# Performance work log

Hardware: AMD Instinct MI355X
Metric: run time of the kernel (lower is better)

Reference implementation:

```python
import jax, jax.numpy as jnp
import numpy as np

S, W = 256, 64          # sentences per doc, words per sentence
V, E = 100000, 256      # vocab, embedding dim
HW, HS, C = 256, 256, 10  # word hidden, sentence hidden, num categories


def _gru_dir(x, Wih, Whh, bih, bhh, reverse):
    """Single-direction GRU, PyTorch gate order (r, z, n). x: [B, T, D] -> [B, T, H]."""
    B, T, D = x.shape
    H = Whh.shape[1]
    xg = jnp.einsum('btd,gd->tbg', x, Wih) + bih  # [T, B, 3H], precompute input gates

    def step(h, xt):
        hg = h @ Whh.T + bhh
        xr, xz, xn = jnp.split(xt, 3, axis=-1)
        hr, hz, hn = jnp.split(hg, 3, axis=-1)
        r = jax.nn.sigmoid(xr + hr)
        z = jax.nn.sigmoid(xz + hz)
        n = jnp.tanh(xn + r * hn)
        h_new = (1.0 - z) * n + z * h
        return h_new, h_new

    h0 = jnp.zeros((B, H), x.dtype)
    _, ys = jax.lax.scan(step, h0, xg, reverse=reverse)  # ys: [T, B, H] in time order
    return jnp.swapaxes(ys, 0, 1)


def _bi_gru(x, WihF, WhhF, bihF, bhhF, WihB, WhhB, bihB, bhhB):
    out_f = _gru_dir(x, WihF, WhhF, bihF, bhhF, reverse=False)
    out_b = _gru_dir(x, WihB, WhhB, bihB, bhhB, reverse=True)
    return jnp.concatenate([out_f, out_b], axis=-1)  # [B, T, 2H]


def _attn_pool(out, w, b):
    # Sequential(Linear(2H,1), Tanh) then softmax over seq dim, weighted sum
    scores = jnp.tanh(out @ w + b)           # [B, T, 1]
    a = jax.nn.softmax(scores, axis=1)       # softmax over time
    return jnp.sum(a * out, axis=1)          # [B, 2H]


def setup_inputs() -> dict:
    key = jax.random.key(0)
    ks = jax.random.split(key, 32)
    sc = 0.05
    d = {
        'tokens': jax.random.randint(ks[0], (S, W), 0, V),
        'emb': jax.random.normal(ks[1], (V, E), jnp.float32) * sc,
        'wWihF': jax.random.normal(ks[2], (3 * HW, E), jnp.float32) * sc,
        'wWhhF': jax.random.normal(ks[3], (3 * HW, HW), jnp.float32) * sc,
        'wBihF': jax.random.normal(ks[4], (3 * HW,), jnp.float32) * sc,
        'wBhhF': jax.random.normal(ks[5], (3 * HW,), jnp.float32) * sc,
        'wWihB': jax.random.normal(ks[6], (3 * HW, E), jnp.float32) * sc,
        'wWhhB': jax.random.normal(ks[7], (3 * HW, HW), jnp.float32) * sc,
        'wBihB': jax.random.normal(ks[8], (3 * HW,), jnp.float32) * sc,
        'wBhhB': jax.random.normal(ks[9], (3 * HW,), jnp.float32) * sc,
        'sWihF': jax.random.normal(ks[10], (3 * HS, 2 * HW), jnp.float32) * sc,
        'sWhhF': jax.random.normal(ks[11], (3 * HS, HS), jnp.float32) * sc,
        'sBihF': jax.random.normal(ks[12], (3 * HS,), jnp.float32) * sc,
        'sBhhF': jax.random.normal(ks[13], (3 * HS,), jnp.float32) * sc,
        'sWihB': jax.random.normal(ks[14], (3 * HS, 2 * HW), jnp.float32) * sc,
        'sWhhB': jax.random.normal(ks[15], (3 * HS, HS), jnp.float32) * sc,
        'sBihB': jax.random.normal(ks[16], (3 * HS,), jnp.float32) * sc,
        'sBhhB': jax.random.normal(ks[17], (3 * HS,), jnp.float32) * sc,
        'wAttW': jax.random.normal(ks[18], (2 * HW, 1), jnp.float32) * sc,
        'wAttB': jax.random.normal(ks[19], (1,), jnp.float32) * sc,
        'sAttW': jax.random.normal(ks[20], (2 * HS, 1), jnp.float32) * sc,
        'sAttB': jax.random.normal(ks[21], (1,), jnp.float32) * sc,
        'clsW': jax.random.normal(ks[22], (C, 2 * HS), jnp.float32) * sc,
        'clsB': jax.random.normal(ks[23], (C,), jnp.float32) * sc,
    }
    return d


def reference(tokens, emb, wWihF, wWhhF, wBihF, wBhhF, wWihB, wWhhB, wBihB, wBhhB,
              sWihF, sWhhF, sBihF, sBhhF, sWihB, sWhhB, sBihB, sBhhB,
              wAttW, wAttB, sAttW, sAttB, clsW, clsB):
    # word level: all sentences batched together (packed form of the Python loop)
    x = emb[tokens]                                             # [S, W, E]
    word_out = _bi_gru(x, wWihF, wWhhF, wBihF, wBhhF, wWihB, wWhhB, wBihB, wBhhB)  # [S, W, 2HW]
    sent_vecs = _attn_pool(word_out, wAttW, wAttB)              # [S, 2HW]
    # sentence level: single document
    sent_in = sent_vecs[None]                                   # [1, S, 2HW]
    sent_out = _bi_gru(sent_in, sWihF, sWhhF, sBihF, sBhhF, sWihB, sWhhB, sBihB, sBhhB)  # [1, S, 2HS]
    doc_vec = _attn_pool(sent_out, sAttW, sAttB)                # [1, 2HS]
    logits = doc_vec @ clsW.T + clsB                            # [1, C]
    return jax.nn.softmax(logits, axis=1)
```

## Files before the change

### kernel.cpp

```cpp
#include <hip/hip_runtime.h>
#include <stdint.h>

typedef unsigned short ushort_t;
typedef uint32_t u32;
typedef __bf16 bf16;
typedef bf16 bf16x8 __attribute__((ext_vector_type(8)));
typedef float f32x4 __attribute__((ext_vector_type(4)));
typedef ushort_t ushort8 __attribute__((ext_vector_type(8)));

__device__ __forceinline__ float b2f(ushort_t u) {
    u32 x = ((u32)u) << 16;
    return __builtin_bit_cast(float, x);
}
__device__ __forceinline__ ushort_t f2b(float f) {
    bf16 h = (bf16)f;
    return __builtin_bit_cast(ushort_t, h);
}
__device__ __forceinline__ float sigmoidf_(float x) { return 1.0f / (1.0f + __expf(-x)); }
__device__ __forceinline__ float tanhf_(float x) { return 1.0f - 2.0f / (1.0f + __expf(2.0f * x)); }

__device__ __forceinline__ ushort8 cvt8(const float* __restrict__ p) {
    float4 v0 = *(const float4*)p;
    float4 v1 = *(const float4*)(p + 4);
    ushort8 r;
    r[0] = f2b(v0.x); r[1] = f2b(v0.y); r[2] = f2b(v0.z); r[3] = f2b(v0.w);
    r[4] = f2b(v1.x); r[5] = f2b(v1.y); r[6] = f2b(v1.z); r[7] = f2b(v1.w);
    return r;
}

#define TPAD 40

__global__ __launch_bounds__(256) void gemm_xg(
    const float* __restrict__ A, const int* __restrict__ tok,
    const float* __restrict__ WF, const float* __restrict__ WB,
    const float* __restrict__ bF, const float* __restrict__ bB,
    ushort_t* __restrict__ C, int K)
{
    __shared__ ushort_t aT[128 * TPAD];
    __shared__ ushort_t bT[128 * TPAD];
    const int tid = threadIdx.x;
    const int lane = tid & 63, wv = tid >> 6;
    const int bn0 = blockIdx.x * 128;
    const int rm0 = blockIdx.y * 128;
    const int wm = (wv & 1) * 64, wn = (wv >> 1) * 64;

    f32x4 acc[4][4];
    f32x4 zero = {0.f, 0.f, 0.f, 0.f};
#pragma unroll
    for (int i = 0; i < 4; i++)
#pragma unroll
        for (int j = 0; j < 4; j++) acc[i][j] = zero;

    const int sr = tid >> 1;
    const int sk = (tid & 1) * 16;
    long arow = tok ? (long)tok[rm0 + sr] : (long)(rm0 + sr);
    const float* aSrc = A + arow * K + sk;
    int ng = bn0 + sr;
    const float* bSrc = (ng < 768 ? WF + (long)ng * K : WB + (long)(ng - 768) * K) + sk;

    const int nkc = K / 32;
    const int fm = lane & 15, fq = (lane >> 4) * 8;
    for (int kc = 0; kc < nkc; ++kc) {
        ushort8 av0 = cvt8(aSrc + kc * 32);
        ushort8 av1 = cvt8(aSrc + kc * 32 + 8);
        ushort8 bv0 = cvt8(bSrc + kc * 32);
        ushort8 bv1 = cvt8(bSrc + kc * 32 + 8);
        __syncthreads();
        *(ushort8*)(aT + sr * TPAD + sk) = av0;
        *(ushort8*)(aT + sr * TPAD + sk + 8) = av1;
        *(ushort8*)(bT + sr * TPAD + sk) = bv0;
        *(ushort8*)(bT + sr * TPAD + sk + 8) = bv1;
        __syncthreads();
        bf16x8 af[4], bfg[4];
#pragma unroll
        for (int i = 0; i < 4; i++)
            af[i] = __builtin_bit_cast(bf16x8, *(const ushort8*)(aT + (wm + i * 16 + fm) * TPAD + fq));
#pragma unroll
        for (int j = 0; j < 4; j++)
            bfg[j] = __builtin_bit_cast(bf16x8, *(const ushort8*)(bT + (wn + j * 16 + fm) * TPAD + fq));
#pragma unroll
        for (int i = 0; i < 4; i++)
#pragma unroll
            for (int j = 0; j < 4; j++)
                acc[i][j] = __builtin_amdgcn_mfma_f32_16x16x32_bf16(af[i], bfg[j], acc[i][j], 0, 0, 0);
    }
    const int fr0 = (lane >> 4) * 4;
#pragma unroll
    for (int j = 0; j < 4; j++) {
        int col = bn0 + wn + j * 16 + fm;
        float bias = (col < 768) ? bF[col] : bB[col - 768];
#pragma unroll
        for (int i = 0; i < 4; i++) {
#pragma unroll
            for (int r = 0; r < 4; r++) {
                int row = rm0 + wm + i * 16 + fr0 + r;
                C[(long)row * 1536 + col] = f2b(acc[i][j][r] + bias);
            }
        }
    }
}

#define HBS 264
#define HGS 770

__global__ __launch_bounds__(512, 2) void gru_level(
    const float* __restrict__ WhhF, const float* __restrict__ WhhB,
    const float* __restrict__ bhhF, const float* __restrict__ bhhB,
    const ushort_t* __restrict__ xg,
    ushort_t* __restrict__ out,
    int T, int NS)
{
    __shared__ ushort_t hbf[16 * HBS];
    __shared__ float hg[16 * HGS];
    __shared__ float bhh_l[768];

    const int tid = threadIdx.x, lane = tid & 63, wv = tid >> 6;
    const int dir = blockIdx.x & 1;
    const int grp = blockIdx.x >> 1;
    const float* Whh = dir ? WhhB : WhhF;
    const float* bhh = dir ? bhhB : bhhF;
    const int dirOff = dir * 768;

    const int n0 = wv * 96;
    const int fm = lane & 15, fq = (lane >> 4) * 8;

    bf16x8 wfrag[6][8];
#pragma unroll
    for (int j = 0; j < 6; ++j) {
        const float* wrow = Whh + (long)(n0 + j * 16 + fm) * 256 + fq;
#pragma unroll
        for (int kc = 0; kc < 8; ++kc)
            wfrag[j][kc] = __builtin_bit_cast(bf16x8, cvt8(wrow + kc * 32));
    }
    for (int i = tid; i < 768; i += 512) bhh_l[i] = bhh[i];
    for (int i = tid; i < 16 * HBS / 2; i += 512) ((u32*)hbf)[i] = 0u;

    const int e0 = tid * 2;
    const int um = e0 >> 8;
    const int ud = e0 & 255;
    const bool upd = (e0 < NS * 256);
    float h0 = 0.f, h1 = 0.f;
    const int s = grp * NS + um;
    const ushort_t* xgBase = xg + (long)s * T * 1536 + dirOff + ud;
    ushort_t* outBase = out + (long)s * T * 512 + dir * 256 + ud;
    __syncthreads();

    for (int st = 0; st < T; ++st) {
        const int tt = dir ? (T - 1 - st) : st;
        f32x4 acc[6];
        f32x4 zero = {0.f, 0.f, 0.f, 0.f};
#pragma unroll
        for (int j = 0; j < 6; ++j) acc[j] = zero;
#pragma unroll
        for (int kc = 0; kc < 8; ++kc) {
            bf16x8 a = __builtin_bit_cast(bf16x8, *(const ushort8*)(hbf + fm * HBS + kc * 32 + fq));
#pragma unroll
            for (int j = 0; j < 6; ++j)
                acc[j] = __builtin_amdgcn_mfma_f32_16x16x32_bf16(a, wfrag[j][kc], acc[j], 0, 0, 0);
        }
        const int mr = (lane >> 4) * 4;
#pragma unroll
        for (int j = 0; j < 6; ++j) {
            int col = n0 + j * 16 + fm;
#pragma unroll
            for (int r = 0; r < 4; ++r) {
                int m = mr + r;
                if (m < NS) hg[m * HGS + col] = acc[j][r];
            }
        }
        __syncthreads();
        if (upd) {
            float hr0 = hg[um * HGS + ud] + bhh_l[ud];
            float hr1 = hg[um * HGS + ud + 1] + bhh_l[ud + 1];
            float hz0 = hg[um * HGS + 256 + ud] + bhh_l[256 + ud];
            float hz1 = hg[um * HGS + 256 + ud + 1] + bhh_l[256 + ud + 1];
            float hn0 = hg[um * HGS + 512 + ud] + bhh_l[512 + ud];
            float hn1 = hg[um * HGS + 512 + ud + 1] + bhh_l[512 + ud + 1];
            const ushort_t* xp = xgBase + (long)tt * 1536;
            u32 xr = *(const u32*)(xp);
            u32 xz = *(const u32*)(xp + 256);
            u32 xn = *(const u32*)(xp + 512);
            float r0 = sigmoidf_(b2f((ushort_t)xr) + hr0);
            float r1 = sigmoidf_(b2f((ushort_t)(xr >> 16)) + hr1);
            float z0 = sigmoidf_(b2f((ushort_t)xz) + hz0);
            float z1 = sigmoidf_(b2f((ushort_t)(xz >> 16)) + hz1);
            float nn0 = tanhf_(b2f((ushort_t)xn) + r0 * hn0);
            float nn1 = tanhf_(b2f((ushort_t)(xn >> 16)) + r1 * hn1);
            h0 = (1.f - z0) * nn0 + z0 * h0;
            h1 = (1.f - z1) * nn1 + z1 * h1;
            u32 hb = (u32)f2b(h0) | ((u32)f2b(h1) << 16);
            *(u32*)(hbf + um * HBS + ud) = hb;
            *(u32*)(outBase + (long)tt * 512) = hb;
        }
        __syncthreads();
    }
}

__global__ void attn_word(const ushort_t* __restrict__ wout,
                          const float* __restrict__ attW,
                          const float* __restrict__ attB,
                          float* __restrict__ svec)
{
    __shared__ float part[64][4];
    __shared__ float aw[64];
    const int s = blockIdx.x, tid = threadIdx.x;
    const int w = tid >> 2, q = tid & 3;
    const ushort_t* row = wout + ((long)(s * 64 + w)) * 512 + q * 128;
    const float* ap = attW + q * 128;
    float sum = 0.f;
    for (int i = 0; i < 128; i += 8) {
        ushort8 a = *(const ushort8*)(row + i);
        float4 b0 = *(const float4*)(ap + i);
        float4 b1 = *(const float4*)(ap + i + 4);
        sum += b2f(a[0]) * b0.x + b2f(a[1]) * b0.y + b2f(a[2]) * b0.z + b2f(a[3]) * b0.w
             + b2f(a[4]) * b1.x + b2f(a[5]) * b1.y + b2f(a[6]) * b1.z + b2f(a[7]) * b1.w;
    }
    part[w][q] = sum;
    __syncthreads();
    if (tid < 64) {
        float sc = tanhf_(part[tid][0] + part[tid][1] + part[tid][2] + part[tid][3] + attB[0]);
        float m = sc;
#pragma unroll
        for (int o = 32; o >= 1; o >>= 1) m = fmaxf(m, __shfl_xor(m, o, 64));
        float e = __expf(sc - m);
        float se = e;
#pragma unroll
        for (int o = 32; o >= 1; o >>= 1) se += __shfl_xor(se, o, 64);
        aw[tid] = e / se;
    }
    __syncthreads();
    const int d = tid * 2;
    float a0 = 0.f, a1 = 0.f;
    const ushort_t* col = wout + ((long)(s * 64)) * 512 + d;
#pragma unroll 4
    for (int w2 = 0; w2 < 64; ++w2) {
        u32 v = *(const u32*)(col + (long)w2 * 512);
        float wg = aw[w2];
        a0 += wg * b2f((ushort_t)v);
        a1 += wg * b2f((ushort_t)(v >> 16));
    }
    *(float2*)(svec + (long)s * 512 + d) = make_float2(a0, a1);
}

__global__ void attn_sent(const ushort_t* __restrict__ sout,
                          const float* __restrict__ attW,
                          const float* __restrict__ attB,
                          float* __restrict__ doc)
{
    __shared__ float aw[256];
    __shared__ float red[8];
    const int tid = threadIdx.x;
    const ushort_t* row = sout + (long)tid * 512;
    float sum = 0.f;
    for (int i = 0; i < 512; i += 8) {
        ushort8 a = *(const ushort8*)(row + i);
        float4 b0 = *(const float4*)(attW + i);
        float4 b1 = *(const float4*)(attW + i + 4);
        sum += b2f(a[0]) * b0.x + b2f(a[1]) * b0.y + b2f(a[2]) * b0.z + b2f(a[3]) * b0.w
             + b2f(a[4]) * b1.x + b2f(a[5]) * b1.y + b2f(a[6]) * b1.z + b2f(a[7]) * b1.w;
    }
    float sc = tanhf_(sum + attB[0]);
    float m = sc;
#pragma unroll
    for (int o = 32; o >= 1; o >>= 1) m = fmaxf(m, __shfl_xor(m, o, 64));
    if ((tid & 63) == 0) red[tid >> 6] = m;
    __syncthreads();
    m = fmaxf(fmaxf(red[0], red[1]), fmaxf(red[2], red[3]));
    float e = __expf(sc - m);
    float se = e;
#pragma unroll
    for (int o = 32; o >= 1; o >>= 1) se += __shfl_xor(se, o, 64);
    if ((tid & 63) == 0) red[4 + (tid >> 6)] = se;
    __syncthreads();
    se = red[4] + red[5] + red[6] + red[7];
    aw[tid] = e / se;
    __syncthreads();
    const int d = tid * 2;
    float a0 = 0.f, a1 = 0.f;
    for (int t2 = 0; t2 < 256; ++t2) {
        u32 v = *(const u32*)(sout + (long)t2 * 512 + d);
        float w = aw[t2];
        a0 += w * b2f((ushort_t)v);
        a1 += w * b2f((ushort_t)(v >> 16));
    }
    doc[d] = a0;
    doc[d + 1] = a1;
}

__global__ void classify(const float* __restrict__ doc, const float* __restrict__ clsW,
                         const float* __restrict__ clsB, float* __restrict__ outp)
{
    const int lane = threadIdx.x;
    float logit = -1e30f;
    if (lane < 10) {
        float s = clsB[lane];
        const float* wr = clsW + lane * 512;
        for (int i = 0; i < 512; ++i) s += doc[i] * wr[i];
        logit = s;
    }
    float m = logit;
#pragma unroll
    for (int o = 32; o >= 1; o >>= 1) m = fmaxf(m, __shfl_xor(m, o, 64));
    float e = (lane < 10) ? __expf(logit - m) : 0.f;
    float se = e;
#pragma unroll
    for (int o = 32; o >= 1; o >>= 1) se += __shfl_xor(se, o, 64);
    if (lane < 10) outp[lane] = e / se;
}

extern "C" void kernel_launch(void* const* d_in, const int* in_sizes, int n_in,
                              void* d_out, int out_size, void* d_ws, size_t ws_size,
                              hipStream_t stream)
{
    const int*   tokens = (const int*)d_in[0];
    const float* emb    = (const float*)d_in[1];
    const float* wWihF  = (const float*)d_in[2];
    const float* wWhhF  = (const float*)d_in[3];
    const float* wBihF  = (const float*)d_in[4];
    const float* wBhhF  = (const float*)d_in[5];
    const float* wWihB  = (const float*)d_in[6];
    const float* wWhhB  = (const float*)d_in[7];
    const float* wBihB  = (const float*)d_in[8];
    const float* wBhhB  = (const float*)d_in[9];
    const float* sWihF  = (const float*)d_in[10];
    const float* sWhhF  = (const float*)d_in[11];
    const float* sBihF  = (const float*)d_in[12];
    const float* sBhhF  = (const float*)d_in[13];
    const float* sWihB  = (const float*)d_in[14];
    const float* sWhhB  = (const float*)d_in[15];
    const float* sBihB  = (const float*)d_in[16];
    const float* sBhhB  = (const float*)d_in[17];
    const float* wAttW  = (const float*)d_in[18];
    const float* wAttB  = (const float*)d_in[19];
    const float* sAttW  = (const float*)d_in[20];
    const float* sAttB  = (const float*)d_in[21];
    const float* clsW   = (const float*)d_in[22];
    const float* clsB   = (const float*)d_in[23];

    char* ws = (char*)d_ws;
    ushort_t* xg   = (ushort_t*)(ws);
    ushort_t* wout = (ushort_t*)(ws + 50331648);
    float*    svec = (float*)(ws + 67108864);
    ushort_t* sxg  = (ushort_t*)(ws + 67633152);
    ushort_t* sout = (ushort_t*)(ws + 68419584);
    float*    doc  = (float*)(ws + 68681728);

    gemm_xg<<<dim3(12, 128), 256, 0, stream>>>(emb, tokens, wWihF, wWihB, wBihF, wBihB, xg, 256);
    gru_level<<<128, 512, 0, stream>>>(wWhhF, wWhhB, wBhhF, wBhhB, xg, wout, 64, 4);
    attn_word<<<256, 256, 0, stream>>>(wout, wAttW, wAttB, svec);
    gemm_xg<<<dim3(12, 2), 256, 0, stream>>>(svec, nullptr, sWihF, sWihB, sBihF, sBihB, sxg, 512);
    gru_level<<<2, 512, 0, stream>>>(sWhhF, sWhhB, sBhhF, sBhhB, sxg, sout, 256, 1);
    attn_sent<<<1, 256, 0, stream>>>(sout, sAttW, sAttB, doc);
    classify<<<1, 64, 0, stream>>>(doc, clsW, clsB, (float*)d_out);
}
```

Before: 890.1 us.

## Fuse GRU gate update into MFMA epilogue with double-buffered hidden state

Each wave now owns matching r/z/n columns for its 32 hidden units, so the gate nonlinearity and state update run straight from MFMA accumulators instead of going through a shared hg buffer. The hidden state is double-buffered, which allows one barrier per step instead of two. Next-step xg values are prefetched into registers and output writes are deferred by one step. The word-level pass now runs 2 sentences per block over 256 blocks instead of 4 over 128, which spreads the sequential work across more CUs. The cost is more registers, and only one lane group of each wave does the elementwise work.

```diff
diff --git a/kernel.cpp b/kernel.cpp
--- a/kernel.cpp
+++ b/kernel.cpp
@@ -101,18 +101,16 @@
 }
 
 #define HBS 264
-#define HGS 770
-
+
+template<int NS>
 __global__ __launch_bounds__(512, 2) void gru_level(
     const float* __restrict__ WhhF, const float* __restrict__ WhhB,
     const float* __restrict__ bhhF, const float* __restrict__ bhhB,
     const ushort_t* __restrict__ xg,
     ushort_t* __restrict__ out,
-    int T, int NS)
-{
-    __shared__ ushort_t hbf[16 * HBS];
-    __shared__ float hg[16 * HGS];
-    __shared__ float bhh_l[768];
+    int T)
+{
+    __shared__ ushort_t hbf[2][16 * HBS];
 
     const int tid = threadIdx.x, lane = tid & 63, wv = tid >> 6;
     const int dir = blockIdx.x & 1;
@@ -121,78 +119,114 @@
     const float* bhh = dir ? bhhB : bhhF;
     const int dirOff = dir * 768;
 
-    const int n0 = wv * 96;
     const int fm = lane & 15, fq = (lane >> 4) * 8;
+    const int mgrp = lane >> 4;
+    const int d0 = 32 * wv + fm;
 
     bf16x8 wfrag[6][8];
 #pragma unroll
-    for (int j = 0; j < 6; ++j) {
-        const float* wrow = Whh + (long)(n0 + j * 16 + fm) * 256 + fq;
-#pragma unroll
-        for (int kc = 0; kc < 8; ++kc)
-            wfrag[j][kc] = __builtin_bit_cast(bf16x8, cvt8(wrow + kc * 32));
-    }
-    for (int i = tid; i < 768; i += 512) bhh_l[i] = bhh[i];
-    for (int i = tid; i < 16 * HBS / 2; i += 512) ((u32*)hbf)[i] = 0u;
-
-    const int e0 = tid * 2;
-    const int um = e0 >> 8;
-    const int ud = e0 & 255;
-    const bool upd = (e0 < NS * 256);
-    float h0 = 0.f, h1 = 0.f;
-    const int s = grp * NS + um;
-    const ushort_t* xgBase = xg + (long)s * T * 1536 + dirOff + ud;
-    ushort_t* outBase = out + (long)s * T * 512 + dir * 256 + ud;
+    for (int g = 0; g < 3; ++g)
+#pragma unroll
+        for (int t = 0; t < 2; ++t) {
+            const float* wrow = Whh + (long)(g * 256 + 32 * wv + 16 * t + fm) * 256 + fq;
+#pragma unroll
+            for (int kc = 0; kc < 8; ++kc)
+                wfrag[g * 2 + t][kc] = __builtin_bit_cast(bf16x8, cvt8(wrow + kc * 32));
+        }
+
+    float bhhv[3][2];
+#pragma unroll
+    for (int g = 0; g < 3; ++g)
+#pragma unroll
+        for (int t = 0; t < 2; ++t)
+            bhhv[g][t] = bhh[g * 256 + d0 + 16 * t];
+
+    for (int i = tid; i < 16 * HBS; i += 512) { hbf[0][i] = 0; hbf[1][i] = 0; }
+
+    const ushort_t* xgm[NS];
+    ushort_t* outm[NS];
+#pragma unroll
+    for (int m = 0; m < NS; ++m) {
+        int s = grp * NS + m;
+        xgm[m] = xg + (long)s * T * 1536 + dirOff;
+        outm[m] = out + (long)s * T * 512 + dir * 256;
+    }
+
+    float h[NS][2];
+    ushort_t xv[NS][3][2];
+    ushort_t ostage[NS][2];
+#pragma unroll
+    for (int m = 0; m < NS; ++m) { h[m][0] = 0.f; h[m][1] = 0.f; }
+
+    if (mgrp == 0) {
+        const int tt0 = dir ? (T - 1) : 0;
+#pragma unroll
+        for (int m = 0; m < NS; ++m)
+#pragma unroll
+            for (int g = 0; g < 3; ++g)
+#pragma unroll
+                for (int t = 0; t < 2; ++t)
+                    xv[m][g][t] = xgm[m][(long)tt0 * 1536 + g * 256 + d0 + 16 * t];
+    }
     __syncthreads();
 
     for (int st = 0; st < T; ++st) {
-        const int tt = dir ? (T - 1 - st) : st;
+        const int cur = st & 1, nxt = cur ^ 1;
+        if (st > 0 && mgrp == 0) {
+            const int tp = dir ? (T - st) : (st - 1);
+#pragma unroll
+            for (int m = 0; m < NS; ++m) {
+                outm[m][(long)tp * 512 + d0] = ostage[m][0];
+                outm[m][(long)tp * 512 + d0 + 16] = ostage[m][1];
+            }
+        }
         f32x4 acc[6];
         f32x4 zero = {0.f, 0.f, 0.f, 0.f};
 #pragma unroll
-        for (int j = 0; j < 6; ++j) acc[j] = zero;
+        for (int gi = 0; gi < 6; ++gi) acc[gi] = zero;
 #pragma unroll
         for (int kc = 0; kc < 8; ++kc) {
-            bf16x8 a = __builtin_bit_cast(bf16x8, *(const ushort8*)(hbf + fm * HBS + kc * 32 + fq));
-#pragma unroll
-            for (int j = 0; j < 6; ++j)
-                acc[j] = __builtin_amdgcn_mfma_f32_16x16x32_bf16(a, wfrag[j][kc], acc[j], 0, 0, 0);
-        }
-        const int mr = (lane >> 4) * 4;
-#pragma unroll
-        for (int j = 0; j < 6; ++j) {
-            int col = n0 + j * 16 + fm;
-#pragma unroll
-            for (int r = 0; r < 4; ++r) {
-                int m = mr + r;
-                if (m < NS) hg[m * HGS + col] = acc[j][r];
-            }
+            bf16x8 a = __builtin_bit_cast(bf16x8,
+                *(const ushort8*)(&hbf[cur][fm * HBS + kc * 32 + fq]));
+#pragma unroll
+            for (int gi = 0; gi < 6; ++gi)
+                acc[gi] = __builtin_amdgcn_mfma_f32_16x16x32_bf16(a, wfrag[gi][kc], acc[gi], 0, 0, 0);
+        }
+        if (mgrp == 0) {
+#pragma unroll
+            for (int m = 0; m < NS; ++m)
+#pragma unroll
+                for (int t = 0; t < 2; ++t) {
+                    float xr = b2f(xv[m][0][t]);
+                    float xz = b2f(xv[m][1][t]);
+                    float xn = b2f(xv[m][2][t]);
+                    float r = sigmoidf_(xr + acc[0 + t][m] + bhhv[0][t]);
+                    float z = sigmoidf_(xz + acc[2 + t][m] + bhhv[1][t]);
+                    float n = tanhf_(xn + r * (acc[4 + t][m] + bhhv[2][t]));
+                    h[m][t] = (1.f - z) * n + z * h[m][t];
+                    ushort_t hb = f2b(h[m][t]);
+                    hbf[nxt][m * HBS + d0 + 16 * t] = hb;
+                    ostage[m][t] = hb;
+                }
+            const int stn = (st + 1 < T) ? (st + 1) : st;
+            const int ttn = dir ? (T - 1 - stn) : stn;
+#pragma unroll
+            for (int m = 0; m < NS; ++m)
+#pragma unroll
+                for (int g = 0; g < 3; ++g)
+#pragma unroll
+                    for (int t = 0; t < 2; ++t)
+                        xv[m][g][t] = xgm[m][(long)ttn * 1536 + g * 256 + d0 + 16 * t];
         }
         __syncthreads();
-        if (upd) {
-            float hr0 = hg[um * HGS + ud] + bhh_l[ud];
-            float hr1 = hg[um * HGS + ud + 1] + bhh_l[ud + 1];
-            float hz0 = hg[um * HGS + 256 + ud] + bhh_l[256 + ud];
-            float hz1 = hg[um * HGS + 256 + ud + 1] + bhh_l[256 + ud + 1];
-            float hn0 = hg[um * HGS + 512 + ud] + bhh_l[512 + ud];
-            float hn1 = hg[um * HGS + 512 + ud + 1] + bhh_l[512 + ud + 1];
-            const ushort_t* xp = xgBase + (long)tt * 1536;
-            u32 xr = *(const u32*)(xp);
-            u32 xz = *(const u32*)(xp + 256);
-            u32 xn = *(const u32*)(xp + 512);
-            float r0 = sigmoidf_(b2f((ushort_t)xr) + hr0);
-            float r1 = sigmoidf_(b2f((ushort_t)(xr >> 16)) + hr1);
-            float z0 = sigmoidf_(b2f((ushort_t)xz) + hz0);
-            float z1 = sigmoidf_(b2f((ushort_t)(xz >> 16)) + hz1);
-            float nn0 = tanhf_(b2f((ushort_t)xn) + r0 * hn0);
-            float nn1 = tanhf_(b2f((ushort_t)(xn >> 16)) + r1 * hn1);
-            h0 = (1.f - z0) * nn0 + z0 * h0;
-            h1 = (1.f - z1) * nn1 + z1 * h1;
-            u32 hb = (u32)f2b(h0) | ((u32)f2b(h1) << 16);
-            *(u32*)(hbf + um * HBS + ud) = hb;
-            *(u32*)(outBase + (long)tt * 512) = hb;
-        }
-        __syncthreads();
+    }
+    if (mgrp == 0) {
+        const int tl = dir ? 0 : (T - 1);
+#pragma unroll
+        for (int m = 0; m < NS; ++m) {
+            outm[m][(long)tl * 512 + d0] = ostage[m][0];
+            outm[m][(long)tl * 512 + d0 + 16] = ostage[m][1];
+        }
     }
 }
 
@@ -346,10 +380,10 @@
     float*    doc  = (float*)(ws + 68681728);
 
     gemm_xg<<<dim3(12, 128), 256, 0, stream>>>(emb, tokens, wWihF, wWihB, wBihF, wBihB, xg, 256);
-    gru_level<<<128, 512, 0, stream>>>(wWhhF, wWhhB, wBhhF, wBhhB, xg, wout, 64, 4);
+    gru_level<2><<<256, 512, 0, stream>>>(wWhhF, wWhhB, wBhhF, wBhhB, xg, wout, 64);
     attn_word<<<256, 256, 0, stream>>>(wout, wAttW, wAttB, svec);
     gemm_xg<<<dim3(12, 2), 256, 0, stream>>>(svec, nullptr, sWihF, sWihB, sBihF, sBihB, sxg, 512);
-    gru_level<<<2, 512, 0, stream>>>(sWhhF, sWhhB, sBhhF, sBhhB, sxg, sout, 256, 1);
+    gru_level<1><<<2, 512, 0, stream>>>(sWhhF, sWhhB, sBhhF, sBhhB, sxg, sout, 256);
     attn_sent<<<1, 256, 0, stream>>>(sout, sAttW, sAttB, doc);
     classify<<<1, 64, 0, stream>>>(doc, clsW, clsB, (float*)d_out);
 }
```

After: 951.0 us. +6.8%, slower.
